# Optimization experiments

Hardware: AMD Instinct MI355X
Metric: run time of the kernel (lower is better)

## Reference

```python
import jax, jax.numpy as jnp
import numpy as np

N, E, IN, H, C = 20000, 320000, 512, 4, 64
HC = H * C
EPS_BN = 1e-5


def setup_inputs() -> dict:
    key = jax.random.key(0)
    ks = jax.random.split(key, 12)
    p = lambda k, shape, s=0.05: jax.random.normal(k, shape, dtype=jnp.float32) * s
    z = lambda n: jnp.zeros((n,), jnp.float32)
    o = lambda n: jnp.ones((n,), jnp.float32)
    return {
        "x": jax.random.normal(ks[0], (N, IN), dtype=jnp.float32),
        "edge_index": jax.random.randint(ks[1], (2, E), 0, N),
        "Wl0": p(ks[2], (IN, HC)), "Wr0": p(ks[3], (IN, HC)),
        "att0": p(ks[4], (H, C)), "b0": z(HC),
        "g0": o(HC), "be0": z(HC), "m0": z(HC), "v0": o(HC),
        "Wl1": p(ks[5], (HC, HC)), "Wr1": p(ks[6], (HC, HC)),
        "att1": p(ks[7], (H, C)), "b1": z(HC),
        "g1": o(HC), "be1": z(HC), "m1": z(HC), "v1": o(HC),
        "Wl2": p(ks[8], (HC, 2)), "Wr2": p(ks[9], (HC, 2)),
        "att2": p(ks[10], (1, 2)), "b2": z(2),
    }


def gatv2_conv(x, Wl, Wr, att, b, ei, concat):
    # GATv2: e_ij = att . LeakyReLU(Wl x_j + Wr x_i); softmax over in-edges of i
    n = x.shape[0]
    h, c = att.shape
    xl = (x @ Wl).reshape(n, h, c)  # source/message transform
    xr = (x @ Wr).reshape(n, h, c)  # target transform
    src, dst = ei[0], ei[1]
    m = xl[src] + xr[dst]                                   # [E,H,C] edge gather
    e = jnp.sum(jax.nn.leaky_relu(m, 0.2) * att, axis=-1)   # [E,H]
    emax = jax.ops.segment_max(e, dst, num_segments=n)      # segment softmax
    emax = jnp.where(jnp.isfinite(emax), emax, 0.0)
    ex = jnp.exp(e - emax[dst])
    denom = jax.ops.segment_sum(ex, dst, num_segments=n)
    alpha = ex / (denom[dst] + 1e-16)                       # [E,H]
    out = jax.ops.segment_sum(alpha[:, :, None] * xl[src], dst, num_segments=n)
    out = out.reshape(n, h * c) if concat else out.mean(axis=1)
    return out + b


def bn_eval(x, g, be, m, v):
    return (x - m) * (g * jax.lax.rsqrt(v + EPS_BN)) + be


def reference(x, edge_index, Wl0, Wr0, att0, b0, g0, be0, m0, v0,
              Wl1, Wr1, att1, b1, g1, be1, m1, v1, Wl2, Wr2, att2, b2):
    loops = jnp.arange(N)
    ei = jnp.concatenate([edge_index, jnp.stack([loops, loops])], axis=1)
    h = gatv2_conv(x, Wl0, Wr0, att0, b0, ei, True)
    h = jax.nn.elu(bn_eval(h, g0, be0, m0, v0))
    h = gatv2_conv(h, Wl1, Wr1, att1, b1, ei, True)
    h = jax.nn.elu(bn_eval(h, g1, be1, m1, v1))
    out = gatv2_conv(h, Wl2, Wr2, att2, b2, ei, False)
    return jax.nn.log_softmax(out, axis=1)
```

## Files before the change

### kernel.cpp

```cpp
#include <hip/hip_runtime.h>
#include <math.h>

#define NN 20000
#define MP 20096
#define EE 320000
#define ET (EE + NN)
#define HC 256
#define EPS_BN 1e-5f

typedef __bf16 bf16x8 __attribute__((ext_vector_type(8)));
typedef float f32x4 __attribute__((ext_vector_type(4)));

__device__ __forceinline__ float4 ld4(const float* p) { return *reinterpret_cast<const float4*>(p); }
__device__ __forceinline__ float lrelu(float x) { return fmaxf(x, 0.f) + 0.2f * fminf(x, 0.f); }

__device__ __forceinline__ unsigned short f2b(float f) {
  unsigned int u = __float_as_uint(f);
  u = (u + 0x7fffu + ((u >> 16) & 1u)) >> 16;
  return (unsigned short)u;
}
__device__ __forceinline__ float b2f(unsigned short u) {
  return __uint_as_float(((unsigned int)u) << 16);
}

__device__ __forceinline__ void gld_lds16(const void* g, void* l) {
  __builtin_amdgcn_global_load_lds(
      (const __attribute__((address_space(1))) unsigned int*)g,
      (__attribute__((address_space(3))) unsigned int*)(unsigned int)(unsigned long long)l,
      16, 0, 0);
}

__global__ __launch_bounds__(256) void convert_x_kernel(const float* __restrict__ x,
                                                        unsigned short* __restrict__ xb) {
  int i = (blockIdx.x * 256 + threadIdx.x) * 4;
  if (i >= NN * 512) return;
  float4 v = ld4(&x[i]);
  ushort4 o;
  o.x = f2b(v.x); o.y = f2b(v.y); o.z = f2b(v.z); o.w = f2b(v.w);
  *reinterpret_cast<ushort4*>(&xb[i]) = o;
}

__global__ __launch_bounds__(256) void convert_w_kernel(const float* __restrict__ Wl,
                                                        const float* __restrict__ Wr,
                                                        unsigned short* __restrict__ Wf,
                                                        int K) {
  int idx = blockIdx.x * 256 + threadIdx.x;
  if (idx >= 512 * K) return;
  int n = idx / K, k = idx - n * K;
  float v = (n < 256) ? Wl[(size_t)k * 256 + n] : Wr[(size_t)k * 256 + (n - 256)];
  Wf[idx] = f2b(v);
}

__global__ __launch_bounds__(256) void gemm_mfma(const unsigned short* __restrict__ A,
                                                 const unsigned short* __restrict__ Bt,
                                                 unsigned short* __restrict__ xlb,
                                                 float* __restrict__ xrf,
                                                 int M, int K) {
  __shared__ unsigned short As[128 * 32];
  __shared__ unsigned short Bs[128 * 32];
  const int wave = threadIdx.x >> 6;
  const int lane = threadIdx.x & 63;
  const int am = lane & 15;
  const int aq = lane >> 4;
  const int wr = (wave >> 1) * 64;
  const int wc = (wave & 1) * 64;
  const int row0 = blockIdx.y * 128;
  const int col0 = blockIdx.x * 128;

  f32x4 acc[4][4] = {};

  for (int kk = 0; kk < K; kk += 32) {
    __syncthreads();
#pragma unroll
    for (int c = 0; c < 2; ++c) {
      int seg = wave * 128 + c * 64 + lane;
      int r = seg >> 2, ks = (seg & 3) * 8;
      gld_lds16(A + (size_t)(row0 + r) * K + kk + ks, &As[(wave * 128 + c * 64) * 8]);
      gld_lds16(Bt + (size_t)(col0 + r) * K + kk + ks, &Bs[(wave * 128 + c * 64) * 8]);
    }
    __syncthreads();

    bf16x8 af[4], bfr[4];
#pragma unroll
    for (int i = 0; i < 4; ++i)
      af[i] = *reinterpret_cast<const bf16x8*>(&As[(wr + i * 16 + am) * 32 + aq * 8]);
#pragma unroll
    for (int j = 0; j < 4; ++j)
      bfr[j] = *reinterpret_cast<const bf16x8*>(&Bs[(wc + j * 16 + am) * 32 + aq * 8]);
#pragma unroll
    for (int i = 0; i < 4; ++i)
#pragma unroll
      for (int j = 0; j < 4; ++j)
        acc[i][j] = __builtin_amdgcn_mfma_f32_16x16x32_bf16(af[i], bfr[j], acc[i][j], 0, 0, 0);
  }

#pragma unroll
  for (int i = 0; i < 4; ++i) {
#pragma unroll
    for (int j = 0; j < 4; ++j) {
      int gcol = col0 + wc + j * 16 + am;
#pragma unroll
      for (int rr = 0; rr < 4; ++rr) {
        int grow = row0 + wr + i * 16 + aq * 4 + rr;
        if (grow < M) {
          float v = acc[i][j][rr];
          if (gcol < 256) xlb[(size_t)grow * 256 + gcol] = f2b(v);
          else            xrf[(size_t)grow * 256 + (gcol - 256)] = v;
        }
      }
    }
  }
}

__global__ __launch_bounds__(256) void hist_kernel(const int* __restrict__ ei,
                                                   int* __restrict__ counts) {
  int e = blockIdx.x * blockDim.x + threadIdx.x;
  if (e >= ET) return;
  int d = (e < EE) ? ei[EE + e] : (e - EE);
  atomicAdd(&counts[d], 1);
}

__global__ __launch_bounds__(1024) void scan_kernel(int* __restrict__ cursor,
                                                    int* __restrict__ offsets) {
  __shared__ int wsum[16];
  const int tid = threadIdx.x;
  const int lane = tid & 63, wv = tid >> 6;
  const int base = tid * 20;
  int vals[20];
  int s = 0;
  if (tid < 1000) {
#pragma unroll
    for (int j = 0; j < 20; ++j) { vals[j] = cursor[base + j]; s += vals[j]; }
  }
  int ssum = s;
#pragma unroll
  for (int off = 1; off < 64; off <<= 1) {
    int t = __shfl_up(ssum, off);
    if (lane >= off) ssum += t;
  }
  if (lane == 63) wsum[wv] = ssum;
  __syncthreads();
  if (wv == 0) {
    int w = (lane < 16) ? wsum[lane] : 0;
#pragma unroll
    for (int off = 1; off < 16; off <<= 1) {
      int t = __shfl_up(w, off);
      if (lane >= off) w += t;
    }
    if (lane < 16) wsum[lane] = w;
  }
  __syncthreads();
  int excl = ssum - s + (wv > 0 ? wsum[wv - 1] : 0);
  if (tid < 1000) {
    int run = excl;
#pragma unroll
    for (int j = 0; j < 20; ++j) { offsets[base + j] = run; cursor[base + j] = run; run += vals[j]; }
  }
  if (tid == 1023) offsets[NN] = wsum[15];
}

__global__ __launch_bounds__(256) void scatter_kernel(const int* __restrict__ ei,
                                                      int* __restrict__ cursor,
                                                      int* __restrict__ srcs) {
  int e = blockIdx.x * blockDim.x + threadIdx.x;
  if (e >= ET) return;
  int s, d;
  if (e < EE) { s = ei[e]; d = ei[EE + e]; } else { s = d = e - EE; }
  int pos = atomicAdd(&cursor[d], 1);
  srcs[pos] = s;
}

__global__ __launch_bounds__(256) void gat_layer(const unsigned short* __restrict__ xlb,
                                                 const float* __restrict__ xrf,
                                                 const float* __restrict__ att,
                                                 const float* __restrict__ bias,
                                                 const float* __restrict__ gam,
                                                 const float* __restrict__ bet,
                                                 const float* __restrict__ mean,
                                                 const float* __restrict__ var,
                                                 const int* __restrict__ offsets,
                                                 const int* __restrict__ srcs,
                                                 unsigned short* __restrict__ hb) {
  const int wave = threadIdx.x >> 6;
  const int lane = threadIdx.x & 63;
  const int node = blockIdx.x * 4 + wave;
  if (node >= NN) return;

  const float4 xr4 = ld4(&xrf[(size_t)node * HC + lane * 4]);
  const float4 a4 = ld4(&att[lane * 4]);
  const int beg = offsets[node];
  const int end = offsets[node + 1];

  float lA = 0.f, lB = 0.f;
  float4 OA = make_float4(0.f, 0.f, 0.f, 0.f);
  float4 OB = make_float4(0.f, 0.f, 0.f, 0.f);

  int i = beg;
  for (; i + 3 < end; i += 4) {
    int s0 = srcs[i], s1 = srcs[i + 1], s2 = srcs[i + 2], s3 = srcs[i + 3];
    ushort4 u0 = *reinterpret_cast<const ushort4*>(&xlb[(size_t)s0 * HC + lane * 4]);
    ushort4 u1 = *reinterpret_cast<const ushort4*>(&xlb[(size_t)s1 * HC + lane * 4]);
    ushort4 u2 = *reinterpret_cast<const ushort4*>(&xlb[(size_t)s2 * HC + lane * 4]);
    ushort4 u3 = *reinterpret_cast<const ushort4*>(&xlb[(size_t)s3 * HC + lane * 4]);
    float4 x0 = make_float4(b2f(u0.x), b2f(u0.y), b2f(u0.z), b2f(u0.w));
    float4 x1 = make_float4(b2f(u1.x), b2f(u1.y), b2f(u1.z), b2f(u1.w));
    float4 x2 = make_float4(b2f(u2.x), b2f(u2.y), b2f(u2.z), b2f(u2.w));
    float4 x3 = make_float4(b2f(u3.x), b2f(u3.y), b2f(u3.z), b2f(u3.w));
    float e0 = lrelu(x0.x + xr4.x) * a4.x + lrelu(x0.y + xr4.y) * a4.y +
               lrelu(x0.z + xr4.z) * a4.z + lrelu(x0.w + xr4.w) * a4.w;
    float e1 = lrelu(x1.x + xr4.x) * a4.x + lrelu(x1.y + xr4.y) * a4.y +
               lrelu(x1.z + xr4.z) * a4.z + lrelu(x1.w + xr4.w) * a4.w;
    float e2 = lrelu(x2.x + xr4.x) * a4.x + lrelu(x2.y + xr4.y) * a4.y +
               lrelu(x2.z + xr4.z) * a4.z + lrelu(x2.w + xr4.w) * a4.w;
    float e3 = lrelu(x3.x + xr4.x) * a4.x + lrelu(x3.y + xr4.y) * a4.y +
               lrelu(x3.z + xr4.z) * a4.z + lrelu(x3.w + xr4.w) * a4.w;
#pragma unroll
    for (int off = 1; off < 16; off <<= 1) {
      e0 += __shfl_xor(e0, off);
      e1 += __shfl_xor(e1, off);
      e2 += __shfl_xor(e2, off);
      e3 += __shfl_xor(e3, off);
    }
    float p0 = __expf(e0), p1 = __expf(e1), p2 = __expf(e2), p3 = __expf(e3);
    lA += p0; lB += p1; lA += p2; lB += p3;
    OA.x += p0 * x0.x; OA.y += p0 * x0.y; OA.z += p0 * x0.z; OA.w += p0 * x0.w;
    OB.x += p1 * x1.x; OB.y += p1 * x1.y; OB.z += p1 * x1.z; OB.w += p1 * x1.w;
    OA.x += p2 * x2.x; OA.y += p2 * x2.y; OA.z += p2 * x2.z; OA.w += p2 * x2.w;
    OB.x += p3 * x3.x; OB.y += p3 * x3.y; OB.z += p3 * x3.z; OB.w += p3 * x3.w;
  }
  for (; i < end; ++i) {
    int s = srcs[i];
    ushort4 u = *reinterpret_cast<const ushort4*>(&xlb[(size_t)s * HC + lane * 4]);
    float4 x0 = make_float4(b2f(u.x), b2f(u.y), b2f(u.z), b2f(u.w));
    float e = lrelu(x0.x + xr4.x) * a4.x + lrelu(x0.y + xr4.y) * a4.y +
              lrelu(x0.z + xr4.z) * a4.z + lrelu(x0.w + xr4.w) * a4.w;
#pragma unroll
    for (int off = 1; off < 16; off <<= 1) e += __shfl_xor(e, off);
    float p = __expf(e);
    lA += p;
    OA.x += p * x0.x; OA.y += p * x0.y; OA.z += p * x0.z; OA.w += p * x0.w;
  }
  float inv = 1.f / (lA + lB);
  float4 O = make_float4(OA.x + OB.x, OA.y + OB.y, OA.z + OB.z, OA.w + OB.w);

  float4 b4 = ld4(&bias[lane * 4]);
  float4 g4 = ld4(&gam[lane * 4]);
  float4 e4 = ld4(&bet[lane * 4]);
  float4 m4 = ld4(&mean[lane * 4]);
  float4 v4 = ld4(&var[lane * 4]);
  float y0 = O.x * inv + b4.x, y1 = O.y * inv + b4.y;
  float y2 = O.z * inv + b4.z, y3 = O.w * inv + b4.w;
  float z0 = (y0 - m4.x) * (g4.x * rsqrtf(v4.x + EPS_BN)) + e4.x;
  float z1 = (y1 - m4.y) * (g4.y * rsqrtf(v4.y + EPS_BN)) + e4.y;
  float z2 = (y2 - m4.z) * (g4.z * rsqrtf(v4.z + EPS_BN)) + e4.z;
  float z3 = (y3 - m4.w) * (g4.w * rsqrtf(v4.w + EPS_BN)) + e4.w;
  ushort4 r;
  r.x = f2b(z0 > 0.f ? z0 : expm1f(z0));
  r.y = f2b(z1 > 0.f ? z1 : expm1f(z1));
  r.z = f2b(z2 > 0.f ? z2 : expm1f(z2));
  r.w = f2b(z3 > 0.f ? z3 : expm1f(z3));
  *reinterpret_cast<ushort4*>(&hb[(size_t)node * HC + lane * 4]) = r;
}

__global__ __launch_bounds__(256) void lin2_kernel(const unsigned short* __restrict__ hb,
                                                   const float* __restrict__ Wl,
                                                   const float* __restrict__ Wr,
                                                   float* __restrict__ xl2,
                                                   float* __restrict__ xr2) {
  const int wave = threadIdx.x >> 6;
  const int lane = threadIdx.x & 63;
  const int node = blockIdx.x * 4 + wave;
  if (node >= NN) return;
  ushort4 h4 = *reinterpret_cast<const ushort4*>(&hb[(size_t)node * HC + lane * 4]);
  float hv[4] = {b2f(h4.x), b2f(h4.y), b2f(h4.z), b2f(h4.w)};
  float l0 = 0.f, l1 = 0.f, r0 = 0.f, r1 = 0.f;
#pragma unroll
  for (int j = 0; j < 4; ++j) {
    int row = lane * 4 + j;
    l0 += hv[j] * Wl[row * 2 + 0];
    l1 += hv[j] * Wl[row * 2 + 1];
    r0 += hv[j] * Wr[row * 2 + 0];
    r1 += hv[j] * Wr[row * 2 + 1];
  }
#pragma unroll
  for (int off = 1; off < 64; off <<= 1) {
    l0 += __shfl_xor(l0, off);
    l1 += __shfl_xor(l1, off);
    r0 += __shfl_xor(r0, off);
    r1 += __shfl_xor(r1, off);
  }
  if (lane == 0) {
    xl2[node * 2 + 0] = l0; xl2[node * 2 + 1] = l1;
    xr2[node * 2 + 0] = r0; xr2[node * 2 + 1] = r1;
  }
}

__global__ __launch_bounds__(256) void gat2_out_kernel(const float* __restrict__ xl2,
                                                       const float* __restrict__ xr2,
                                                       const float* __restrict__ att2,
                                                       const float* __restrict__ b2,
                                                       const int* __restrict__ offsets,
                                                       const int* __restrict__ srcs,
                                                       float* __restrict__ out) {
  const int wave = threadIdx.x >> 6;
  const int lane = threadIdx.x & 63;
  const int node = blockIdx.x * 4 + wave;
  if (node >= NN) return;
  const float a0 = att2[0], a1 = att2[1];
  const float xr0 = xr2[node * 2 + 0], xr1 = xr2[node * 2 + 1];
  const int beg = offsets[node], end = offsets[node + 1];

  float l = 0.f, o0 = 0.f, o1 = 0.f;
  for (int i = beg + lane; i < end; i += 64) {
    int s = srcs[i];
    float x0 = xl2[s * 2 + 0], x1 = xl2[s * 2 + 1];
    float e = lrelu(x0 + xr0) * a0 + lrelu(x1 + xr1) * a1;
    float p = __expf(e);
    l += p;
    o0 += p * x0;
    o1 += p * x1;
  }
#pragma unroll
  for (int off = 1; off < 64; off <<= 1) {
    l += __shfl_xor(l, off);
    o0 += __shfl_xor(o0, off);
    o1 += __shfl_xor(o1, off);
  }
  if (lane == 0) {
    float inv = 1.f / l;
    float t0 = o0 * inv + b2[0];
    float t1 = o1 * inv + b2[1];
    float mx = fmaxf(t0, t1);
    float ls = mx + logf(__expf(t0 - mx) + __expf(t1 - mx));
    out[node * 2 + 0] = t0 - ls;
    out[node * 2 + 1] = t1 - ls;
  }
}

extern "C" void kernel_launch(void* const* d_in, const int* in_sizes, int n_in,
                              void* d_out, int out_size, void* d_ws, size_t ws_size,
                              hipStream_t stream) {
  const float* x    = (const float*)d_in[0];
  const int*   ei   = (const int*)d_in[1];
  const float* Wl0  = (const float*)d_in[2];
  const float* Wr0  = (const float*)d_in[3];
  const float* att0 = (const float*)d_in[4];
  const float* b0   = (const float*)d_in[5];
  const float* g0   = (const float*)d_in[6];
  const float* be0  = (const float*)d_in[7];
  const float* m0   = (const float*)d_in[8];
  const float* v0   = (const float*)d_in[9];
  const float* Wl1  = (const float*)d_in[10];
  const float* Wr1  = (const float*)d_in[11];
  const float* att1 = (const float*)d_in[12];
  const float* b1   = (const float*)d_in[13];
  const float* g1   = (const float*)d_in[14];
  const float* be1  = (const float*)d_in[15];
  const float* m1   = (const float*)d_in[16];
  const float* v1   = (const float*)d_in[17];
  const float* Wl2  = (const float*)d_in[18];
  const float* Wr2  = (const float*)d_in[19];
  const float* att2 = (const float*)d_in[20];
  const float* b2   = (const float*)d_in[21];

  float* xrf = (float*)d_ws;
  unsigned short* xlb = (unsigned short*)(xrf + (size_t)NN * 256);
  unsigned short* hb  = xlb + (size_t)NN * 256;
  unsigned short* xb  = hb + (size_t)MP * 256;
  unsigned short* Wf0 = xb + (size_t)MP * 512;
  unsigned short* Wf1 = Wf0 + 512 * 512;
  float* xl2 = (float*)(Wf1 + 512 * 256);
  float* xr2 = xl2 + 2 * NN;
  int* offsets = (int*)(xr2 + 2 * NN);
  int* cursor  = offsets + (NN + 1);
  int* srcs    = cursor + NN;

  hipMemsetAsync(cursor, 0, NN * sizeof(int), stream);
  hist_kernel<<<(ET + 255) / 256, 256, 0, stream>>>(ei, cursor);
  convert_x_kernel<<<(NN * 512 / 4 + 255) / 256, 256, 0, stream>>>(x, xb);
  convert_w_kernel<<<(512 * 512 + 255) / 256, 256, 0, stream>>>(Wl0, Wr0, Wf0, 512);
  convert_w_kernel<<<(512 * 256 + 255) / 256, 256, 0, stream>>>(Wl1, Wr1, Wf1, 256);
  scan_kernel<<<1, 1024, 0, stream>>>(cursor, offsets);
  scatter_kernel<<<(ET + 255) / 256, 256, 0, stream>>>(ei, cursor, srcs);

  dim3 gemm_grid(4, MP / 128);
  gemm_mfma<<<gemm_grid, 256, 0, stream>>>(xb, Wf0, xlb, xrf, NN, 512);
  gat_layer<<<NN / 4, 256, 0, stream>>>(xlb, xrf, att0, b0, g0, be0, m0, v0, offsets, srcs, hb);
  gemm_mfma<<<gemm_grid, 256, 0, stream>>>(hb, Wf1, xlb, xrf, NN, 256);
  gat_layer<<<NN / 4, 256, 0, stream>>>(xlb, xrf, att1, b1, g1, be1, m1, v1, offsets, srcs, hb);
  lin2_kernel<<<NN / 4, 256, 0, stream>>>(hb, Wl2, Wr2, xl2, xr2);
  gat2_out_kernel<<<NN / 4, 256, 0, stream>>>(xl2, xr2, att2, b2, offsets, srcs, (float*)d_out);
}
```

Baseline: 304.2 us.

## Multi-buffer GEMM LDS tiles with prefetch two k-steps ahead

Turns the single-buffered LDS tiles of the bf16 MFMA GEMM into a 4-slot ring and issues direct global-to-LDS loads two k-tiles ahead. Explicit vmcnt waits and one barrier per iteration replace the two __syncthreads per k-step. The aim is to hide global load latency behind MFMA work. In exchange the kernel uses 4x the LDS (64 KB), which may lower occupancy, and correctness depends on the hand-tuned vmcnt counts.

```diff
diff --git a/kernel.cpp b/kernel.cpp
--- a/kernel.cpp
+++ b/kernel.cpp
@@ -56,8 +56,8 @@
                                                  unsigned short* __restrict__ xlb,
                                                  float* __restrict__ xrf,
                                                  int M, int K) {
-  __shared__ unsigned short As[128 * 32];
-  __shared__ unsigned short Bs[128 * 32];
+  __shared__ unsigned short As[4][128 * 32];
+  __shared__ unsigned short Bs[4][128 * 32];
   const int wave = threadIdx.x >> 6;
   const int lane = threadIdx.x & 63;
   const int am = lane & 15;
@@ -67,32 +67,57 @@
   const int row0 = blockIdx.y * 128;
   const int col0 = blockIdx.x * 128;
 
+  const int seg0 = wave * 128 + lane;
+  const int r0 = seg0 >> 2, k0 = (seg0 & 3) * 8;
+  const int seg1 = seg0 + 64;
+  const int r1 = seg1 >> 2, k1 = (seg1 & 3) * 8;
+  const size_t aoff0 = (size_t)(row0 + r0) * K + k0;
+  const size_t aoff1 = (size_t)(row0 + r1) * K + k1;
+  const size_t boff0 = (size_t)(col0 + r0) * K + k0;
+  const size_t boff1 = (size_t)(col0 + r1) * K + k1;
+
+  const int nk = K >> 5;
+
+#define STAGE(tt, bb)                                                      \
+  do {                                                                     \
+    gld_lds16(A + aoff0 + (size_t)(tt) * 32, &As[bb][(wave * 128) * 8]);   \
+    gld_lds16(Bt + boff0 + (size_t)(tt) * 32, &Bs[bb][(wave * 128) * 8]);  \
+    gld_lds16(A + aoff1 + (size_t)(tt) * 32, &As[bb][(wave * 128 + 64) * 8]); \
+    gld_lds16(Bt + boff1 + (size_t)(tt) * 32, &Bs[bb][(wave * 128 + 64) * 8]); \
+  } while (0)
+
   f32x4 acc[4][4] = {};
 
-  for (int kk = 0; kk < K; kk += 32) {
-    __syncthreads();
-#pragma unroll
-    for (int c = 0; c < 2; ++c) {
-      int seg = wave * 128 + c * 64 + lane;
-      int r = seg >> 2, ks = (seg & 3) * 8;
-      gld_lds16(A + (size_t)(row0 + r) * K + kk + ks, &As[(wave * 128 + c * 64) * 8]);
-      gld_lds16(Bt + (size_t)(col0 + r) * K + kk + ks, &Bs[(wave * 128 + c * 64) * 8]);
+  STAGE(0, 0);
+  STAGE(1, 1);
+
+  for (int t = 0; t < nk; ++t) {
+    const int cur = t & 3;
+    if (t + 2 < nk) {
+      STAGE(t + 2, (t + 2) & 3);
+      asm volatile("s_waitcnt vmcnt(8)" ::: "memory");
+    } else if (t + 1 < nk) {
+      asm volatile("s_waitcnt vmcnt(4)" ::: "memory");
+    } else {
+      asm volatile("s_waitcnt vmcnt(0)" ::: "memory");
     }
-    __syncthreads();
+    __builtin_amdgcn_s_barrier();
+    __builtin_amdgcn_sched_barrier(0);
 
     bf16x8 af[4], bfr[4];
 #pragma unroll
     for (int i = 0; i < 4; ++i)
-      af[i] = *reinterpret_cast<const bf16x8*>(&As[(wr + i * 16 + am) * 32 + aq * 8]);
+      af[i] = *reinterpret_cast<const bf16x8*>(&As[cur][(wr + i * 16 + am) * 32 + aq * 8]);
 #pragma unroll
     for (int j = 0; j < 4; ++j)
-      bfr[j] = *reinterpret_cast<const bf16x8*>(&Bs[(wc + j * 16 + am) * 32 + aq * 8]);
+      bfr[j] = *reinterpret_cast<const bf16x8*>(&Bs[cur][(wc + j * 16 + am) * 32 + aq * 8]);
 #pragma unroll
     for (int i = 0; i < 4; ++i)
 #pragma unroll
       for (int j = 0; j < 4; ++j)
         acc[i][j] = __builtin_amdgcn_mfma_f32_16x16x32_bf16(af[i], bfr[j], acc[i][j], 0, 0, 0);
   }
+#undef STAGE
 
 #pragma unroll
   for (int i = 0; i < 4; ++i) {
```

Result: no change. 308.8 us (+1.5%).
